# Performance work log

Hardware: AMD Instinct MI355X
Metric: run time of the kernel (lower is better)

Reference implementation:

```python
import jax, jax.numpy as jnp
import numpy as np

B, T, D = 2, 2048, 1024
H, HS = 16, 64  # n_head, head_size; H*HS == D
THETA = 10000.0


def setup_inputs() -> dict:
    key = jax.random.key(0)
    ks = jax.random.split(key, 10)
    s = 0.02
    return {
        "x": jax.random.normal(ks[0], (B, T, D), jnp.float32),
        "attention_mask": jnp.ones((B, T), jnp.int32),
        # weights stored [in, out] (transposed torch Linear weight)
        "Wq": jax.random.normal(ks[1], (D, H * HS), jnp.float32) * s,
        "bq": jax.random.normal(ks[2], (H * HS,), jnp.float32) * s,
        "Wk": jax.random.normal(ks[3], (D, H * HS), jnp.float32) * s,
        "bk": jax.random.normal(ks[4], (H * HS,), jnp.float32) * s,
        "Wv": jax.random.normal(ks[5], (D, H * HS), jnp.float32) * s,
        "bv": jax.random.normal(ks[6], (H * HS,), jnp.float32) * s,
        "Wo": jax.random.normal(ks[7], (H * HS, D), jnp.float32) * s,
        "bo": jax.random.normal(ks[8], (D,), jnp.float32) * s,
    }


def _rotate_half(x):
    x1, x2 = x[..., : HS // 2], x[..., HS // 2:]
    return jnp.concatenate((-x2, x1), axis=-1)


def _rope_tables(seq_len, dtype):
    inv_freq = 1.0 / (THETA ** (jnp.arange(0, HS, 2, dtype=jnp.float32) / HS))
    t = jnp.arange(seq_len, dtype=jnp.float32)
    freqs = t[:, None] * inv_freq[None, :]            # [T, HS/2]
    emb = jnp.concatenate((freqs, freqs), axis=-1)    # [T, HS]
    return jnp.cos(emb).astype(dtype), jnp.sin(emb).astype(dtype)


def attention_fwd(x, attention_mask, Wq, bq, Wk, bk, Wv, bv, Wo, bo):
    b, t, c = x.shape
    # QKV projections -> [B, H, T, HS]
    q = (x @ Wq + bq).reshape(b, t, H, HS).transpose(0, 2, 1, 3)
    k = (x @ Wk + bk).reshape(b, t, H, HS).transpose(0, 2, 1, 3)
    v = (x @ Wv + bv).reshape(b, t, H, HS).transpose(0, 2, 1, 3)
    # rotary embedding
    cos, sin = _rope_tables(t, x.dtype)               # [T, HS]
    q = q * cos + _rotate_half(q) * sin
    k = k * cos + _rotate_half(k) * sin
    # expanded causal+padding mask: mask[:,None,None,:] expanded to [B,1,T,T] then tril
    causal = jnp.tril(jnp.ones((t, t), dtype=bool))
    keep = (attention_mask[:, None, None, :] != 0) & causal[None, None]  # [B,1,T,T]
    scale = 1.0 / np.sqrt(HS)
    scores = jnp.einsum('bhqd,bhkd->bhqk', q, k) * scale
    scores = jnp.where(keep, scores, jnp.finfo(scores.dtype).min)
    att = jax.nn.softmax(scores, axis=-1)
    y = jnp.einsum('bhqk,bhkd->bhqd', att, v)         # [B,H,T,HS]
    y = y.transpose(0, 2, 1, 3).reshape(b, t, H * HS)
    return y @ Wo + bo


def reference(x, attention_mask, Wq, bq, Wk, bk, Wv, bv, Wo, bo):
    return attention_fwd(x, attention_mask, Wq, bq, Wk, bk, Wv, bv, Wo, bo)
```

## Files before the change

kernel.cpp:

```cpp
#include <hip/hip_runtime.h>

#define T_SEQ 2048
#define NB 2
#define NH 16
#define HS 64
#define DMODEL 1024
#define NEG_BIG (-3.0e38f)

typedef __attribute__((ext_vector_type(8))) short bf16x8;
typedef __attribute__((ext_vector_type(4))) float f32x4;
#define MFMA16 __builtin_amdgcn_mfma_f32_16x16x32_bf16

__device__ __forceinline__ float bfu2f(unsigned int u) {
    union { unsigned int i; float f; } z; z.i = u << 16; return z.f;
}
__device__ __forceinline__ unsigned short f2bfu(float f) {
    union { float f; unsigned int i; } z; z.f = f;
    unsigned int x = z.i;
    unsigned int r = x + 0x7fffu + ((x >> 16) & 1u);
    return (unsigned short)(r >> 16);
}
__device__ __forceinline__ unsigned int pack_bf16(float a, float b) {
    union { float f; unsigned int u; } x, y; x.f = a; y.f = b;
    return __builtin_amdgcn_perm(y.u + 0x8000u, x.u + 0x8000u, 0x07060302u);
}
__device__ __forceinline__ unsigned int cvtpk_bf16(float a, float b) {
    unsigned int r;
    asm("v_cvt_pk_bf16_f32 %0, %1, %2" : "=v"(r) : "v"(a), "v"(b));
    return r;
}
__device__ __forceinline__ void gl2lds16(const unsigned short* g, unsigned short* l) {
    __builtin_amdgcn_global_load_lds(
        (const __attribute__((address_space(1))) unsigned int*)g,
        (__attribute__((address_space(3))) unsigned int*)l, 16, 0, 0);
}

__global__ __launch_bounds__(256) void prep_kernel(
    const float4* __restrict__ x4, ushort4* __restrict__ o4,
    const float* __restrict__ W0, const float* __restrict__ W1,
    const float* __restrict__ W2, const float* __restrict__ W3,
    unsigned short* __restrict__ T0, unsigned short* __restrict__ T1,
    unsigned short* __restrict__ T2, unsigned short* __restrict__ T3)
{
    const int t = threadIdx.x;
    if (blockIdx.z < 4) {
        __shared__ float tile[32][33];
        const float* W = (blockIdx.z == 0) ? W0 : (blockIdx.z == 1) ? W1 : (blockIdx.z == 2) ? W2 : W3;
        unsigned short* T = (blockIdx.z == 0) ? T0 : (blockIdx.z == 1) ? T1 : (blockIdx.z == 2) ? T2 : T3;
        const int k0 = blockIdx.x * 32, n0 = blockIdx.y * 32;
        const int r = t >> 5, c = t & 31;
        #pragma unroll
        for (int i = 0; i < 4; ++i)
            tile[r + 8 * i][c] = W[(size_t)(k0 + r + 8 * i) * DMODEL + n0 + c];
        __syncthreads();
        #pragma unroll
        for (int i = 0; i < 4; ++i)
            T[(size_t)(n0 + r + 8 * i) * DMODEL + k0 + c] = f2bfu(tile[c][r + 8 * i]);
    } else {
        const int n4 = NB * T_SEQ * DMODEL / 4;
        for (int i = (blockIdx.y * 32 + blockIdx.x) * 256 + t; i < n4; i += 32 * 32 * 256) {
            float4 f = x4[i];
            ushort4 u;
            u.x = f2bfu(f.x); u.y = f2bfu(f.y); u.z = f2bfu(f.z); u.w = f2bfu(f.w);
            o4[i] = u;
        }
    }
}

__global__ __launch_bounds__(256) void qkv_mfma_kernel(
    const unsigned short* __restrict__ A,
    const unsigned short* __restrict__ Wqt, const unsigned short* __restrict__ Wkt,
    const unsigned short* __restrict__ Wvt,
    const float* __restrict__ bq, const float* __restrict__ bk, const float* __restrict__ bv,
    unsigned short* __restrict__ qo, unsigned short* __restrict__ ko,
    unsigned short* __restrict__ vt)
{
    __shared__ unsigned short As[64 * 64];
    __shared__ unsigned short Bs[128 * 64];
    const int tid = threadIdx.x;
    const int wave = tid >> 6, lane = tid & 63;
    const int lane15 = lane & 15, quad = lane >> 4;
    const int sw = lane15 & 7;
    const int z = blockIdx.z;
    const unsigned short* Bt = (z == 0) ? Wqt : (z == 1) ? Wkt : Wvt;
    const float* bias = (z == 0) ? bq : (z == 1) ? bk : bv;
    const int m0 = blockIdx.x * 64, n0 = blockIdx.y * 128;
    const int mh = (wave & 1) * 32, nh = (wave >> 1) * 64;
    const int oks0 = ((0 + quad) ^ sw) * 8;
    const int oks1 = ((4 + quad) ^ sw) * 8;

    f32x4 acc[2][4];
    #pragma unroll
    for (int i = 0; i < 2; ++i)
        #pragma unroll
        for (int j = 0; j < 4; ++j) acc[i][j] = (f32x4){0.f, 0.f, 0.f, 0.f};

    int srow[4], soff[4];
    #pragma unroll
    for (int it = 0; it < 4; ++it) {
        int cc = it * 256 + tid;
        srow[it] = cc >> 3;
        soff[it] = ((cc & 7) ^ (srow[it] & 7)) * 8;
    }

    for (int kk = 0; kk < 16; ++kk) {
        __syncthreads();
        #pragma unroll
        for (int it = 0; it < 2; ++it) {
            int cc = it * 256 + tid;
            gl2lds16(A + (size_t)(m0 + srow[it]) * DMODEL + kk * 64 + soff[it], As + cc * 8);
        }
        #pragma unroll
        for (int it = 0; it < 4; ++it) {
            int cc = it * 256 + tid;
            gl2lds16(Bt + (size_t)(n0 + srow[it]) * DMODEL + kk * 64 + soff[it], Bs + cc * 8);
        }
        __syncthreads();
        #pragma unroll
        for (int ks = 0; ks < 2; ++ks) {
            const int o = ks ? oks1 : oks0;
            bf16x8 af[2], bfr[4];
            #pragma unroll
            for (int i = 0; i < 2; ++i)
                af[i] = *(const bf16x8*)(As + (mh + i * 16 + lane15) * 64 + o);
            #pragma unroll
            for (int j = 0; j < 4; ++j)
                bfr[j] = *(const bf16x8*)(Bs + (nh + j * 16 + lane15) * 64 + o);
            #pragma unroll
            for (int i = 0; i < 2; ++i)
                #pragma unroll
                for (int j = 0; j < 4; ++j)
                    acc[i][j] = MFMA16(af[i], bfr[j], acc[i][j], 0, 0, 0);
        }
    }

    const int n0c = n0 + nh;
    const int head = n0c >> 6;
    const float bj0 = bias[n0c + lane15];
    const float bj1 = bias[n0c + 16 + lane15];
    const float bj2 = bias[n0c + 32 + lane15];
    const float bj3 = bias[n0c + 48 + lane15];

    if (z < 2) {
        unsigned short* outp = (z == 0) ? qo : ko;
        const float osc = (z == 0) ? 0.18033688011112042f : 1.0f;
        const float inv0 = __builtin_exp2f(-(float)(lane15)      * 0.41524101186092029f);
        const float inv1 = __builtin_exp2f(-(float)(lane15 + 16) * 0.41524101186092029f);
        #pragma unroll
        for (int i = 0; i < 2; ++i) {
            #pragma unroll
            for (int r = 0; r < 4; ++r) {
                int tok = m0 + mh + i * 16 + quad * 4 + r;
                int bb = tok >> 11, t = tok & (T_SEQ - 1);
                float a0 = (float)t * inv0, a1 = (float)t * inv1;
                float sn0, cs0, sn1, cs1;
                __sincosf(a0, &sn0, &cs0);
                __sincosf(a1, &sn1, &cs1);
                float v0 = acc[i][0][r] + bj0, v1 = acc[i][1][r] + bj1;
                float v2 = acc[i][2][r] + bj2, v3 = acc[i][3][r] + bj3;
                size_t base = ((size_t)(bb * NH + head) * T_SEQ + t) * HS;
                outp[base + lane15]      = f2bfu((v0 * cs0 - v2 * sn0) * osc);
                outp[base + 16 + lane15] = f2bfu((v1 * cs1 - v3 * sn1) * osc);
                outp[base + 32 + lane15] = f2bfu((v2 * cs0 + v0 * sn0) * osc);
                outp[base + 48 + lane15] = f2bfu((v3 * cs1 + v1 * sn1) * osc);
            }
        }
    } else {
        #pragma unroll
        for (int i = 0; i < 2; ++i) {
            int tok0_ = m0 + mh + i * 16 + quad * 4;
            int bb = tok0_ >> 11, t0 = tok0_ & (T_SEQ - 1);
            #pragma unroll
            for (int j = 0; j < 4; ++j) {
                float bj = (j == 0) ? bj0 : (j == 1) ? bj1 : (j == 2) ? bj2 : bj3;
                ushort4 u;
                u.x = f2bfu(acc[i][j][0] + bj);
                u.y = f2bfu(acc[i][j][1] + bj);
                u.z = f2bfu(acc[i][j][2] + bj);
                u.w = f2bfu(acc[i][j][3] + bj);
                *(ushort4*)(vt + ((size_t)(bb * NH + head) * HS + j * 16 + lane15) * T_SEQ + t0) = u;
            }
        }
    }
}

__global__ __launch_bounds__(256, 2) void attn_mfma_kernel(
    const unsigned short* __restrict__ q,
    const unsigned short* __restrict__ k,
    const unsigned short* __restrict__ vt,
    const int* __restrict__ mask,
    unsigned short* __restrict__ pO,
    float* __restrict__ pl)
{
    __shared__ unsigned short Ks[64 * 64];
    __shared__ unsigned short Vs[64 * 64];
    __shared__ unsigned short Pt[4][16 * 64];
    const int tid = threadIdx.x;
    const int wave = tid >> 6, lane = tid & 63;
    const int lane15 = lane & 15, quad = lane >> 4;
    const int sw = lane15 & 7;
    const int oks0 = ((0 + quad) ^ sw) * 8;
    const int oks1 = ((4 + quad) ^ sw) * 8;
    const int bid = blockIdx.x;
    const int bh = bid & 31;
    const int u = 79 - (bid >> 5);
    int qB, c;
    if (u < 8)       { qB = u;                 c = 0; }
    else if (u < 24) { int t = u - 8;  qB = 8  + (t >> 1); c = t & 1; }
    else if (u < 48) { int t = u - 24; qB = 16 + t / 3;    c = t % 3; }
    else             { int t = u - 48; qB = 24 + (t >> 2); c = t & 3; }
    const int slot = bh * 80 + u;
    const int nc  = (qB + 8) >> 3;
    const int len = (qB + nc) / nc;
    const int kt0 = c * len;
    const int kt1 = (kt0 + len - 1 < qB) ? kt0 + len - 1 : qB;
    const int b = bh >> 4;
    const int q0w = qB * 64 + wave * 16;

    const unsigned short* kbase = k  + (size_t)bh * T_SEQ * HS;
    const unsigned short* vbase = vt + (size_t)bh * HS * T_SEQ;

    bf16x8 qf0, qf1;
    {
        const unsigned short* qrow = q + ((size_t)bh * T_SEQ + q0w + lane15) * HS;
        qf0 = *(const bf16x8*)(qrow + quad * 8);
        qf1 = *(const bf16x8*)(qrow + 32 + quad * 8);
    }

    bf16x8 ones;
    #pragma unroll
    for (int i = 0; i < 8; ++i) ones[i] = (short)0x3F80;

    f32x4 accO[4];
    #pragma unroll
    for (int dt = 0; dt < 4; ++dt) accO[dt] = (f32x4){0.f, 0.f, 0.f, 0.f};
    f32x4 acc_l = (f32x4){0.f, 0.f, 0.f, 0.f};

    int srow[2], soff[2];
    #pragma unroll
    for (int it = 0; it < 2; ++it) {
        int cc = it * 256 + tid;
        srow[it] = cc >> 3;
        soff[it] = ((cc & 7) ^ (srow[it] & 7)) * 8;
    }

    for (int kt = kt0; kt <= kt1; ++kt) {
        const int k0 = kt * 64;
        __syncthreads();
        #pragma unroll
        for (int it = 0; it < 2; ++it) {
            int cc = it * 256 + tid;
            gl2lds16(kbase + (size_t)(k0 + srow[it]) * HS + soff[it], Ks + cc * 8);
            gl2lds16(vbase + (size_t)srow[it] * T_SEQ + k0 + soff[it], Vs + cc * 8);
        }
        unsigned long long bal = __ballot(mask[b * T_SEQ + k0 + lane] != 0);
        __syncthreads();

        f32x4 s[4];
        __builtin_amdgcn_s_setprio(1);
        #pragma unroll
        for (int jt = 0; jt < 4; ++jt) {
            bf16x8 kf0 = *(const bf16x8*)(Ks + (jt * 16 + lane15) * 64 + oks0);
            bf16x8 kf1 = *(const bf16x8*)(Ks + (jt * 16 + lane15) * 64 + oks1);
            f32x4 t_ = (f32x4){0.f, 0.f, 0.f, 0.f};
            t_ = MFMA16(kf0, qf0, t_, 0, 0, 0);
            t_ = MFMA16(kf1, qf1, t_, 0, 0, 0);
            s[jt] = t_;
        }
        __builtin_amdgcn_s_setprio(0);

        const bool need_mask = (k0 + 63 > q0w) || (bal != ~0ull);
        if (need_mask) {
            const int qpos = q0w + lane15;
            #pragma unroll
            for (int jt = 0; jt < 4; ++jt) {
                unsigned int mnib = (unsigned int)(bal >> (jt * 16 + quad * 4)) & 15u;
                #pragma unroll
                for (int r = 0; r < 4; ++r) {
                    int kpos = k0 + jt * 16 + quad * 4 + r;
                    bool ok = (kpos <= qpos) && ((mnib >> r) & 1u);
                    s[jt][r] = ok ? s[jt][r] : NEG_BIG;
                }
            }
        }
        #pragma unroll
        for (int jt = 0; jt < 4; ++jt)
            #pragma unroll
            for (int r = 0; r < 4; ++r)
                s[jt][r] = exp2f(s[jt][r]);

        #pragma unroll
        for (int jt = 0; jt < 4; ++jt) {
            unsigned int p01 = cvtpk_bf16(s[jt][0], s[jt][1]);
            unsigned int p23 = cvtpk_bf16(s[jt][2], s[jt][3]);
            int pchunk = (2 * jt + (quad >> 1)) ^ sw;
            int paddr = lane15 * 64 + pchunk * 8 + (quad & 1) * 4;
            *(uint2*)(&Pt[wave][paddr]) = make_uint2(p01, p23);
        }

        bf16x8 pf0 = *(const bf16x8*)(&Pt[wave][lane15 * 64 + oks0]);
        bf16x8 pf1 = *(const bf16x8*)(&Pt[wave][lane15 * 64 + oks1]);
        __builtin_amdgcn_s_setprio(1);
        #pragma unroll
        for (int dt = 0; dt < 4; ++dt) {
            bf16x8 vf0 = *(const bf16x8*)(Vs + (dt * 16 + lane15) * 64 + oks0);
            bf16x8 vf1 = *(const bf16x8*)(Vs + (dt * 16 + lane15) * 64 + oks1);
            accO[dt] = MFMA16(pf0, vf0, accO[dt], 0, 0, 0);
            accO[dt] = MFMA16(pf1, vf1, accO[dt], 0, 0, 0);
        }
        acc_l = MFMA16(pf0, ones, acc_l, 0, 0, 0);
        acc_l = MFMA16(pf1, ones, acc_l, 0, 0, 0);
        __builtin_amdgcn_s_setprio(0);
    }

    unsigned short* ob = pO + (size_t)slot * 4096;
    #pragma unroll
    for (int r = 0; r < 4; ++r) {
        int row = wave * 16 + quad * 4 + r;
        #pragma unroll
        for (int dt = 0; dt < 4; ++dt)
            ob[row * 64 + dt * 16 + lane15] = f2bfu(accO[dt][r]);
    }
    if (lane15 == 0) {
        #pragma unroll
        for (int r = 0; r < 4; ++r)
            pl[slot * 64 + wave * 16 + quad * 4 + r] = acc_l[r];
    }
}

__global__ __launch_bounds__(256) void attn_combine_kernel(
    const unsigned short* __restrict__ pO, const float* __restrict__ pl,
    unsigned short* __restrict__ y)
{
    const int qB = blockIdx.x, bh = blockIdx.y;
    const int b = bh >> 4, h = bh & 15;
    const int tid = threadIdx.x;
    const int row = tid >> 2, cb = (tid & 3) * 16;
    const int nch = (qB + 8) >> 3;
    const int p = (qB < 8) ? qB : (qB < 16) ? 8 + 2 * (qB - 8)
               : (qB < 24) ? 24 + 3 * (qB - 16) : 48 + 4 * (qB - 24);
    const int slot0 = bh * 80 + p;

    float L = 0.f;
    for (int ch = 0; ch < nch; ++ch) L += pl[(slot0 + ch) * 64 + row];
    const float invL = 1.0f / L;

    float a[16];
    #pragma unroll
    for (int i = 0; i < 16; ++i) a[i] = 0.f;
    for (int ch = 0; ch < nch; ++ch) {
        const unsigned short* o = pO + (size_t)(slot0 + ch) * 4096 + row * 64 + cb;
        #pragma unroll
        for (int j = 0; j < 4; ++j) {
            ushort4 u = *(const ushort4*)(o + j * 4);
            a[j * 4 + 0] += bfu2f(u.x); a[j * 4 + 1] += bfu2f(u.y);
            a[j * 4 + 2] += bfu2f(u.z); a[j * 4 + 3] += bfu2f(u.w);
        }
    }
    unsigned short* yrow = y + (size_t)(b * T_SEQ + qB * 64 + row) * DMODEL + h * HS + cb;
    #pragma unroll
    for (int j = 0; j < 4; ++j) {
        ushort4 o;
        o.x = f2bfu(a[j * 4 + 0] * invL); o.y = f2bfu(a[j * 4 + 1] * invL);
        o.z = f2bfu(a[j * 4 + 2] * invL); o.w = f2bfu(a[j * 4 + 3] * invL);
        *(ushort4*)(yrow + j * 4) = o;
    }
}

__global__ __launch_bounds__(256) void outproj_mfma_kernel(
    const unsigned short* __restrict__ A,
    const unsigned short* __restrict__ Bt,
    const float* __restrict__ bo, float* __restrict__ out)
{
    __shared__ unsigned short As[64 * 64];
    __shared__ unsigned short Bs[128 * 64];
    const int tid = threadIdx.x;
    const int wave = tid >> 6, lane = tid & 63;
    const int lane15 = lane & 15, quad = lane >> 4;
    const int sw = lane15 & 7;
    const int oks0 = ((0 + quad) ^ sw) * 8;
    const int oks1 = ((4 + quad) ^ sw) * 8;
    const int m0 = blockIdx.x * 64, n0 = blockIdx.y * 128;
    const int mh = (wave & 1) * 32, nh = (wave >> 1) * 64;

    f32x4 acc[2][4];
    #pragma unroll
    for (int i = 0; i < 2; ++i)
        #pragma unroll
        for (int j = 0; j < 4; ++j) acc[i][j] = (f32x4){0.f, 0.f, 0.f, 0.f};

    int srow[4], soff[4];
    #pragma unroll
    for (int it = 0; it < 4; ++it) {
        int cc = it * 256 + tid;
        srow[it] = cc >> 3;
        soff[it] = ((cc & 7) ^ (srow[it] & 7)) * 8;
    }

    for (int kk = 0; kk < 16; ++kk) {
        __syncthreads();
        #pragma unroll
        for (int it = 0; it < 2; ++it) {
            int cc = it * 256 + tid;
            gl2lds16(A + (size_t)(m0 + srow[it]) * DMODEL + kk * 64 + soff[it], As + cc * 8);
        }
        #pragma unroll
        for (int it = 0; it < 4; ++it) {
            int cc = it * 256 + tid;
            gl2lds16(Bt + (size_t)(n0 + srow[it]) * DMODEL + kk * 64 + soff[it], Bs + cc * 8);
        }
        __syncthreads();
        #pragma unroll
        for (int ks = 0; ks < 2; ++ks) {
            const int o = ks ? oks1 : oks0;
            bf16x8 af[2], bfr[4];
            #pragma unroll
            for (int i = 0; i < 2; ++i)
                af[i] = *(const bf16x8*)(As + (mh + i * 16 + lane15) * 64 + o);
            #pragma unroll
            for (int j = 0; j < 4; ++j)
                bfr[j] = *(const bf16x8*)(Bs + (nh + j * 16 + lane15) * 64 + o);
            #pragma unroll
            for (int i = 0; i < 2; ++i)
                #pragma unroll
                for (int j = 0; j < 4; ++j)
                    acc[i][j] = MFMA16(af[i], bfr[j], acc[i][j], 0, 0, 0);
        }
    }

    const int n0c = n0 + nh;
    const float bj0 = bo[n0c + lane15];
    const float bj1 = bo[n0c + 16 + lane15];
    const float bj2 = bo[n0c + 32 + lane15];
    const float bj3 = bo[n0c + 48 + lane15];
    #pragma unroll
    for (int i = 0; i < 2; ++i) {
        #pragma unroll
        for (int r = 0; r < 4; ++r) {
            int tok = m0 + mh + i * 16 + quad * 4 + r;
            float* orow = out + (size_t)tok * DMODEL + n0c;
            orow[lane15]      = acc[i][0][r] + bj0;
            orow[16 + lane15] = acc[i][1][r] + bj1;
            orow[32 + lane15] = acc[i][2][r] + bj2;
            orow[48 + lane15] = acc[i][3][r] + bj3;
        }
    }
}

extern "C" void kernel_launch(void* const* d_in, const int* in_sizes, int n_in,
                              void* d_out, int out_size, void* d_ws, size_t ws_size,
                              hipStream_t stream)
{
    const float* x  = (const float*)d_in[0];
    const int* mask = (const int*)d_in[1];
    const float* Wq = (const float*)d_in[2];
    const float* bq = (const float*)d_in[3];
    const float* Wk = (const float*)d_in[4];
    const float* bk = (const float*)d_in[5];
    const float* Wv = (const float*)d_in[6];
    const float* bv = (const float*)d_in[7];
    const float* Wo = (const float*)d_in[8];
    const float* bo = (const float*)d_in[9];

    unsigned short* ws = (unsigned short*)d_ws;
    const size_t M1 = 1024 * 1024;
    unsigned short* qw  = ws;
    unsigned short* kw  = ws + 4 * M1;
    unsigned short* vtw = ws + 8 * M1;
    unsigned short* yw  = ws + 12 * M1;
    unsigned short* Wot = ws + 16 * M1;
    unsigned short* xb  = ws + 17 * M1;
    unsigned short* Wqt = ws + 21 * M1;
    unsigned short* Wkt = ws + 22 * M1;
    unsigned short* Wvt = ws + 23 * M1;
    unsigned short* pO  = ws + 17 * M1;
    float* pl = (float*)(ws + 27 * M1);

    prep_kernel<<<dim3(32, 32, 5), 256, 0, stream>>>(
        (const float4*)x, (ushort4*)xb, Wq, Wk, Wv, Wo, Wqt, Wkt, Wvt, Wot);
    qkv_mfma_kernel<<<dim3(64, 8, 3), 256, 0, stream>>>(
        xb, Wqt, Wkt, Wvt, bq, bk, bv, qw, kw, vtw);
    attn_mfma_kernel<<<2560, 256, 0, stream>>>(
        qw, kw, vtw, mask, pO, pl);
    attn_combine_kernel<<<dim3(32, 32), 256, 0, stream>>>(
        pO, pl, yw);
    outproj_mfma_kernel<<<dim3(64, 8), 256, 0, stream>>>(
        yw, Wot, bo, (float*)d_out);
}
```

Baseline: 188.8 us.

## Double-buffer K/V tiles in LDS and prefetch next tile during compute

The attention kernel now keeps two LDS buffers for K and V. It issues the async global-to-LDS load and the mask read for the next key tile before computing on the current tile. This cuts the per-iteration barriers from two to one and aims to hide global memory latency behind the MFMA work. In exchange LDS use per block rises by 16 KB, and correctness depends on the barrier waiting for the async LDS loads to finish.

Result: no change. 190.4 us (+0.9%).

```diff
diff --git a/kernel.cpp b/kernel.cpp
--- a/kernel.cpp
+++ b/kernel.cpp
@@ -192,8 +192,8 @@
     unsigned short* __restrict__ pO,
     float* __restrict__ pl)
 {
-    __shared__ unsigned short Ks[64 * 64];
-    __shared__ unsigned short Vs[64 * 64];
+    __shared__ unsigned short Ks[2][64 * 64];
+    __shared__ unsigned short Vs[2][64 * 64];
     __shared__ unsigned short Pt[4][16 * 64];
     const int tid = threadIdx.x;
     const int wave = tid >> 6, lane = tid & 63;
@@ -220,6 +220,22 @@
     const unsigned short* kbase = k  + (size_t)bh * T_SEQ * HS;
     const unsigned short* vbase = vt + (size_t)bh * HS * T_SEQ;
 
+    int srow[2], soff[2];
+    #pragma unroll
+    for (int it = 0; it < 2; ++it) {
+        int cc = it * 256 + tid;
+        srow[it] = cc >> 3;
+        soff[it] = ((cc & 7) ^ (srow[it] & 7)) * 8;
+    }
+
+    #pragma unroll
+    for (int it = 0; it < 2; ++it) {
+        int cc = it * 256 + tid;
+        gl2lds16(kbase + (size_t)(kt0 * 64 + srow[it]) * HS + soff[it], &Ks[0][cc * 8]);
+        gl2lds16(vbase + (size_t)srow[it] * T_SEQ + kt0 * 64 + soff[it], &Vs[0][cc * 8]);
+    }
+    int mv = mask[b * T_SEQ + kt0 * 64 + lane];
+
     bf16x8 qf0, qf1;
     {
         const unsigned short* qrow = q + ((size_t)bh * T_SEQ + q0w + lane15) * HS;
@@ -236,32 +252,32 @@
     for (int dt = 0; dt < 4; ++dt) accO[dt] = (f32x4){0.f, 0.f, 0.f, 0.f};
     f32x4 acc_l = (f32x4){0.f, 0.f, 0.f, 0.f};
 
-    int srow[2], soff[2];
-    #pragma unroll
-    for (int it = 0; it < 2; ++it) {
-        int cc = it * 256 + tid;
-        srow[it] = cc >> 3;
-        soff[it] = ((cc & 7) ^ (srow[it] & 7)) * 8;
-    }
+    __syncthreads();
 
     for (int kt = kt0; kt <= kt1; ++kt) {
         const int k0 = kt * 64;
-        __syncthreads();
-        #pragma unroll
-        for (int it = 0; it < 2; ++it) {
-            int cc = it * 256 + tid;
-            gl2lds16(kbase + (size_t)(k0 + srow[it]) * HS + soff[it], Ks + cc * 8);
-            gl2lds16(vbase + (size_t)srow[it] * T_SEQ + k0 + soff[it], Vs + cc * 8);
-        }
-        unsigned long long bal = __ballot(mask[b * T_SEQ + k0 + lane] != 0);
-        __syncthreads();
+        const int cur = (kt - kt0) & 1;
+        const unsigned short* Kc = Ks[cur];
+        const unsigned short* Vc = Vs[cur];
+        const unsigned long long bal = __ballot(mv != 0);
+
+        if (kt < kt1) {
+            const int kn = k0 + 64;
+            mv = mask[b * T_SEQ + kn + lane];
+            #pragma unroll
+            for (int it = 0; it < 2; ++it) {
+                int cc = it * 256 + tid;
+                gl2lds16(kbase + (size_t)(kn + srow[it]) * HS + soff[it], &Ks[cur ^ 1][cc * 8]);
+                gl2lds16(vbase + (size_t)srow[it] * T_SEQ + kn + soff[it], &Vs[cur ^ 1][cc * 8]);
+            }
+        }
 
         f32x4 s[4];
         __builtin_amdgcn_s_setprio(1);
         #pragma unroll
         for (int jt = 0; jt < 4; ++jt) {
-            bf16x8 kf0 = *(const bf16x8*)(Ks + (jt * 16 + lane15) * 64 + oks0);
-            bf16x8 kf1 = *(const bf16x8*)(Ks + (jt * 16 + lane15) * 64 + oks1);
+            bf16x8 kf0 = *(const bf16x8*)(Kc + (jt * 16 + lane15) * 64 + oks0);
+            bf16x8 kf1 = *(const bf16x8*)(Kc + (jt * 16 + lane15) * 64 + oks1);
             f32x4 t_ = (f32x4){0.f, 0.f, 0.f, 0.f};
             t_ = MFMA16(kf0, qf0, t_, 0, 0, 0);
             t_ = MFMA16(kf1, qf1, t_, 0, 0, 0);
@@ -303,14 +319,16 @@
         __builtin_amdgcn_s_setprio(1);
         #pragma unroll
         for (int dt = 0; dt < 4; ++dt) {
-            bf16x8 vf0 = *(const bf16x8*)(Vs + (dt * 16 + lane15) * 64 + oks0);
-            bf16x8 vf1 = *(const bf16x8*)(Vs + (dt * 16 + lane15) * 64 + oks1);
+            bf16x8 vf0 = *(const bf16x8*)(Vc + (dt * 16 + lane15) * 64 + oks0);
+            bf16x8 vf1 = *(const bf16x8*)(Vc + (dt * 16 + lane15) * 64 + oks1);
             accO[dt] = MFMA16(pf0, vf0, accO[dt], 0, 0, 0);
             accO[dt] = MFMA16(pf1, vf1, accO[dt], 0, 0, 0);
         }
         acc_l = MFMA16(pf0, ones, acc_l, 0, 0, 0);
         acc_l = MFMA16(pf1, ones, acc_l, 0, 0, 0);
         __builtin_amdgcn_s_setprio(0);
+
+        __syncthreads();
     }
 
     unsigned short* ob = pO + (size_t)slot * 4096;
```
